# Kernel optimization log

Measured on AMD Instinct MI355X. Metric: run time of the kernel, lower is better.

The kernel has to match this reference:

```python
import jax, jax.numpy as jnp
import numpy as np

D, K, S, H, MID, OUT = 1024, 1024, 1000, 16, 4096, 1000
HD = K // H
EPS = 1e-5


def _posenc(d_model, length):
    pos = jnp.arange(length, dtype=jnp.float32)[:, None]              # [S,1]
    div = jnp.exp(jnp.arange(0, d_model, 2, dtype=jnp.float32) * (-np.log(10000.0) / d_model))
    ang = pos * div                                                   # [S,D/2]
    # interleave sin/cos -> pe[:,0::2]=sin, pe[:,1::2]=cos
    return jnp.stack([jnp.sin(ang), jnp.cos(ang)], axis=-1).reshape(length, d_model)


def _ln2d(x):
    # LayerNorm over last two dims (n_seq, d_dim), no affine
    m = jnp.mean(x, axis=(-2, -1), keepdims=True)
    v = jnp.var(x, axis=(-2, -1), keepdims=True)
    return (x - m) * jax.lax.rsqrt(v + EPS)


def setup_inputs() -> dict:
    key = jax.random.key(0)
    ks = jax.random.split(key, 9)
    sc = lambda fan: 1.0 / np.sqrt(fan)
    return {
        "x":   jax.random.normal(ks[0], (8, S, D), dtype=jnp.float32),
        "Wq":  jax.random.normal(ks[1], (D, K), dtype=jnp.float32) * sc(D),
        "Wk":  jax.random.normal(ks[2], (D, K), dtype=jnp.float32) * sc(D),
        "Wv":  jax.random.normal(ks[3], (D, K), dtype=jnp.float32) * sc(D),
        "Wo":  jax.random.normal(ks[4], (K, D), dtype=jnp.float32) * sc(K),
        "W1":  jax.random.normal(ks[5], (D, MID), dtype=jnp.float32) * sc(D),
        "b1":  jnp.zeros((MID,), dtype=jnp.float32),
        "W2":  jax.random.normal(ks[6], (MID, D), dtype=jnp.float32) * sc(MID),
        "b2":  jnp.zeros((D,), dtype=jnp.float32),
        "Wout": jax.random.normal(ks[7], (D, OUT), dtype=jnp.float32) * sc(D),
    }


def reference(x, Wq, Wk, Wv, Wo, W1, b1, W2, b2, Wout):
    B = x.shape[0]
    x = x + _posenc(D, S)                                   # positional add
    # QKV projections -> [B,H,S,HD]
    def heads(w):
        return jnp.einsum('bsd,dk->bsk', x, w).reshape(B, S, H, HD).transpose(0, 2, 1, 3)
    qs, ksv, vs = heads(Wq), heads(Wk), heads(Wv)
    scaling = HD ** (-0.5)
    scores = jnp.einsum('bhsd,bhtd->bhst', qs, ksv) * scaling
    attn = jax.nn.softmax(scores, axis=-1)
    ctx = jnp.einsum('bhst,bhtd->bhsd', attn, vs)
    ctx = ctx.transpose(0, 2, 1, 3).reshape(B, S, K)
    attn_out = _ln2d(jnp.einsum('bsk,kd->bsd', ctx, Wo))    # per-sample LN over (S,D)
    # FFN with residual + LN over (S,D)
    h = jax.nn.relu(jnp.einsum('bsd,dm->bsm', attn_out, W1) + b1)
    f = jnp.einsum('bsm,md->bsd', h, W2) + b2
    ffn = _ln2d(f + attn_out)
    pooled = jnp.mean(ffn, axis=-2)                         # [B,D]
    return jnp.einsum('bd,do->bo', pooled, Wout)            # [B,OUT]
```

## Files before the change

### kernel.cpp

```cpp
#include <hip/hip_runtime.h>
#include <stdint.h>
#include <math.h>

#define DD 1024
#define SS 1000
#define BB 8
#define HH 16
#define MIDD 4096
#define OUTD 1000

typedef unsigned short u16;
typedef __attribute__((ext_vector_type(4))) float f32x4;
typedef __attribute__((ext_vector_type(4))) unsigned int u32x4;

__device__ __forceinline__ u16 f2b(float f) {
    union { float f; uint32_t u; } v; v.f = f;
    uint32_t r = v.u + 0x7fffu + ((v.u >> 16) & 1u);
    return (u16)(r >> 16);
}
__device__ __forceinline__ float b2f(u16 b) {
    union { uint32_t u; float f; } v; v.u = ((uint32_t)b) << 16; return v.f;
}

__device__ __forceinline__ int sz64(int row, int e) {
    return row * 64 + ((((e >> 3) ^ row) & 7) << 3) + (e & 7);
}

__device__ __forceinline__ void mfma_b16(f32x4& d, u32x4 a, u32x4 b) {
    asm("v_mfma_f32_16x16x32_bf16 %0, %1, %2, %0" : "+v"(d) : "v"(a), "v"(b));
}
#define MFMA_FENCE() do { __builtin_amdgcn_sched_barrier(0); \
    asm volatile("s_nop 7\n\ts_nop 7\n\ts_nop 7" ::); \
    __builtin_amdgcn_sched_barrier(0); } while (0)

#define GLDS16(gp, lp) \
    __builtin_amdgcn_global_load_lds((const __attribute__((address_space(1))) uint32_t*)(gp), \
                                     (__attribute__((address_space(3))) uint32_t*)(lp), 16, 0, 0)

__global__ void k_posenc(const float* __restrict__ x, u16* __restrict__ xpe) {
    long p = (long)blockIdx.x * 256 + threadIdx.x;
    if (p >= (long)BB * SS * DD / 2) return;
    int dp = (int)(p & (DD / 2 - 1));
    int s = (int)((p >> 9) % SS);
    float dv = __expf((float)(2 * dp) * (-9.210340371976184f / (float)DD));
    float sn, cs;
    sincosf((float)s * dv, &sn, &cs);
    float2 xv = *(const float2*)&x[p * 2];
    uint32_t pk = (uint32_t)f2b(xv.x + sn) | ((uint32_t)f2b(xv.y + cs) << 16);
    ((uint32_t*)xpe)[p] = pk;
}

__global__ void k_wt(const float* __restrict__ W, u16* __restrict__ Wt, int R, int C, float scale) {
    __shared__ float tile[32][33];
    int bc = blockIdx.x * 32, br = blockIdx.y * 32;
    int tx = threadIdx.x, ty = threadIdx.y;
#pragma unroll
    for (int i = 0; i < 32; i += 8)
        tile[ty + i][tx] = W[(long)(br + ty + i) * C + bc + tx];
    __syncthreads();
#pragma unroll
    for (int i = 0; i < 32; i += 8)
        Wt[(long)(bc + ty + i) * R + br + tx] = f2b(tile[tx][ty + i] * scale);
}

template<int MODE, int BM, bool NFAST>
__global__ __launch_bounds__(512)
void k_gemm(const u16* __restrict__ A, const u16* __restrict__ Bt, void* __restrict__ Cp,
            const float* __restrict__ bias, const u16* res,
            int M, int N, int K, int lda, int ldb, int ldc, int tiles)
{
    constexpr int MF = BM / 32;
    constexpr int AL = BM / 64;
    constexpr int NBUF = (BM == 128) ? 3 : 2;
    __shared__ u16 SA[NBUF][BM * 64];
    __shared__ u16 SB[NBUF][256 * 64];
    const int t = threadIdx.x, lane = t & 63, w = t >> 6;
    const int lr = lane & 15, g = lane >> 4;
    const int wm = w >> 2, wn = w & 3;

    const int orig = blockIdx.x, nwg = gridDim.x;
    const int q8 = nwg >> 3, r8 = nwg & 7, xc = orig & 7;
    const int wg = (xc < r8 ? xc * (q8 + 1) : r8 * (q8 + 1) + (xc - r8) * q8) + (orig >> 3);
    const int bm = (NFAST ? wg / tiles : wg % tiles) * BM;
    const int bn = (NFAST ? wg % tiles : wg / tiles) * 256;

    const int srow8 = lane >> 3;
    const int csrc = ((lane & 7) ^ srow8) << 3;
    const u16* ga[AL];
    const u16* gb[4];
#pragma unroll
    for (int l = 0; l < AL; ++l) {
        int r = bm + w * (BM / 8) + l * 8 + srow8;
        if (r >= M) r = M - 1;
        ga[l] = A + (long)r * lda + csrc;
    }
#pragma unroll
    for (int l = 0; l < 4; ++l)
        gb[l] = Bt + (long)(bn + w * 32 + l * 8 + srow8) * ldb + csrc;

#define STAGE_A(buf, k0) do { \
        _Pragma("unroll") \
        for (int l = 0; l < AL; ++l) \
            GLDS16(ga[l] + (k0), &SA[buf][(w * (BM / 8) + l * 8) * 64]); \
    } while (0)
#define STAGE_B(buf, k0) do { \
        _Pragma("unroll") \
        for (int l = 0; l < 4; ++l) \
            GLDS16(gb[l] + (k0), &SB[buf][(w * 32 + l * 8) * 64]); \
    } while (0)

    f32x4 acc[MF][4] = {};

#define PH(buf, kk) do { \
        u32x4 av[MF], bv[4]; \
        _Pragma("unroll") \
        for (int m = 0; m < MF; ++m) \
            av[m] = *(const u32x4*)&SA[buf][sz64(wm * (BM / 2) + m * 16 + lr, (kk) * 32 + g * 8)]; \
        _Pragma("unroll") \
        for (int n = 0; n < 4; ++n) \
            bv[n] = *(const u32x4*)&SB[buf][sz64(wn * 64 + n * 16 + lr, (kk) * 32 + g * 8)]; \
        __builtin_amdgcn_s_setprio(1); \
        _Pragma("unroll") \
        for (int m = 0; m < MF; ++m) \
            _Pragma("unroll") \
            for (int n = 0; n < 4; ++n) \
                mfma_b16(acc[m][n], av[m], bv[n]); \
        __builtin_amdgcn_s_setprio(0); \
    } while (0)

    const int nt = K >> 6;

    if constexpr (NBUF == 3) {
        STAGE_A(0, 0); STAGE_B(0, 0);
        STAGE_A(1, 64); STAGE_B(1, 64);
        int cb = 0, sb = 2;
        for (int tt = 0; tt < nt; ++tt) {
            if (tt + 1 < nt) asm volatile("s_waitcnt vmcnt(6)" ::: "memory");
            else             asm volatile("s_waitcnt vmcnt(0)" ::: "memory");
            __builtin_amdgcn_s_barrier();
            if (tt + 2 < nt) { STAGE_A(sb, (tt + 2) << 6); STAGE_B(sb, (tt + 2) << 6); }
            PH(cb, 0);
            PH(cb, 1);
            cb = (cb == 2) ? 0 : cb + 1;
            sb = (sb == 2) ? 0 : sb + 1;
        }
    } else {
        STAGE_A(0, 0); STAGE_B(0, 0);
        for (int tt = 0; tt < nt; ++tt) {
            const int cb2 = tt & 1, nb = cb2 ^ 1, kn = (tt + 1) << 6;
            if (tt + 1 < nt) {
                STAGE_A(nb, kn);
                asm volatile("s_waitcnt vmcnt(4)" ::: "memory");
            } else {
                asm volatile("s_waitcnt vmcnt(0)" ::: "memory");
            }
            __builtin_amdgcn_s_barrier();
            PH(cb2, 0);
            if (tt + 1 < nt) STAGE_B(nb, kn);
            PH(cb2, 1);
            __builtin_amdgcn_s_barrier();
        }
    }
#undef PH
#undef STAGE_A
#undef STAGE_B

    MFMA_FENCE();

#pragma unroll
    for (int m = 0; m < MF; ++m) {
#pragma unroll
        for (int j = 0; j < 4; ++j) {
            const int r = bm + wm * (BM / 2) + m * 16 + g * 4 + j;
            if (r >= M) continue;
            const long ro = (long)r * ldc;
#pragma unroll
            for (int n = 0; n < 4; ++n) {
                const int c = bn + wn * 64 + n * 16 + lr;
                float v = acc[m][n][j];
                if (MODE == 0)      ((float*)Cp)[ro + c] = v;
                else if (MODE == 1) ((u16*)Cp)[ro + c] = f2b(v);
                else if (MODE == 2) { v += bias[c]; ((u16*)Cp)[ro + c] = f2b(v > 0.f ? v : 0.f); }
                else                { v += bias[c] + b2f(res[ro + c]); ((u16*)Cp)[ro + c] = f2b(v); }
            }
        }
    }
}

__global__ void k_vt(const u16* __restrict__ QKV, u16* __restrict__ Vt) {
    __shared__ u16 tile[128][80];
    int b = blockIdx.z, h = blockIdx.y, s0 = blockIdx.x * 128;
    int t = threadIdx.x;
    int rr = t >> 3, cc = (t & 7) * 8;
#pragma unroll
    for (int p = 0; p < 4; ++p) {
        int s = s0 + p * 32 + rr;
        uint4 val = make_uint4(0u, 0u, 0u, 0u);
        if (s < SS) val = *(const uint4*)&QKV[((long)(b * SS + s)) * 3072 + 2048 + h * 64 + cc];
        *(uint4*)&tile[p * 32 + rr][cc] = val;
    }
    __syncthreads();
    int d = t >> 2, sg = (t & 3) * 32;
    long base = ((long)((b * HH + h) * 64 + d)) * 1024 + s0 + sg;
#pragma unroll
    for (int i = 0; i < 4; ++i) {
        u16 tmp[8];
#pragma unroll
        for (int jj = 0; jj < 8; ++jj) tmp[jj] = tile[sg + i * 8 + jj][d];
        *(uint4*)&Vt[base + i * 8] = *(uint4*)tmp;
    }
}

__global__ __launch_bounds__(256)
void k_flash(const u16* __restrict__ QKV, const u16* __restrict__ Vt, u16* __restrict__ ctx)
{
    __shared__ u16 Ps[128 * 64];
    __shared__ u16 Ks[64 * 64];
    __shared__ u16 Vs[64 * 64];
    __shared__ u16 Vones[16 * 64];
    const int t = threadIdx.x, lane = t & 63, wave = t >> 6;
    const int lr = lane & 15, g = lane >> 4;
    const int f = blockIdx.x;
    const int bh = (f & 7) + ((f >> 6) << 3);
    const int q0 = ((f >> 3) & 7) * 128;
    const int h = bh & 15, b = bh >> 4;
    const u16* Qg = QKV + (long)b * SS * 3072 + h * 64;
    const u16* Kg = Qg + 1024;
    const u16* Vg = Vt + (long)bh * 65536;

    const int sr8 = wave * 8 + (lane >> 3);
    const int ssrc = ((lane & 7) ^ (lane >> 3)) * 8;
    const int ldst0 = sr8 * 64 + (lane & 7) * 8;
    const int ldst1 = (32 + sr8) * 64 + (lane & 7) * 8;

#pragma unroll
    for (int r = 0; r < 4; ++r) {
        int qr = q0 + r * 32 + sr8; if (qr >= SS) qr = SS - 1;
        GLDS16(Qg + (long)qr * 3072 + ssrc, &Ps[(r * 32 + wave * 8) * 64]);
    }

    u32x4 kr0, kr1, vr0, vr1;
    {
        kr0 = *(const u32x4*)(Kg + (long)sr8 * 3072 + ssrc);
        kr1 = *(const u32x4*)(Kg + (long)(32 + sr8) * 3072 + ssrc);
        vr0 = *(const u32x4*)(Vg + (long)sr8 * 1024 + ssrc);
        vr1 = *(const u32x4*)(Vg + (long)(32 + sr8) * 1024 + ssrc);
    }

    __syncthreads();
    u32x4 qa[2][2];
#pragma unroll
    for (int m = 0; m < 2; ++m)
#pragma unroll
        for (int ks = 0; ks < 2; ++ks)
            qa[m][ks] = *(const u32x4*)&Ps[sz64(wave * 32 + m * 16 + lr, ks * 32 + g * 8)];

    *(u32x4*)&Ks[ldst0] = kr0;
    *(u32x4*)&Ks[ldst1] = kr1;
    *(u32x4*)&Vs[ldst0] = vr0;
    *(u32x4*)&Vs[ldst1] = vr1;
    for (int i = t; i < 16 * 64; i += 256)
        Vones[sz64(i >> 6, i & 63)] = ((i >> 6) == 0) ? (u16)0x3F80 : (u16)0;
    __syncthreads();

    f32x4 o[2][5] = {};

    for (int tt = 0; tt < 16; ++tt) {
        const int kt = tt * 64;
        if (tt < 15) {
            int a0 = kt + 64 + sr8;      if (a0 >= SS) a0 = SS - 1;
            int a1 = kt + 64 + 32 + sr8; if (a1 >= SS) a1 = SS - 1;
            kr0 = *(const u32x4*)(Kg + (long)a0 * 3072 + ssrc);
            kr1 = *(const u32x4*)(Kg + (long)a1 * 3072 + ssrc);
            vr0 = *(const u32x4*)(Vg + (long)sr8 * 1024 + kt + 64 + ssrc);
            vr1 = *(const u32x4*)(Vg + (long)(32 + sr8) * 1024 + kt + 64 + ssrc);
        }

        f32x4 s[2][4] = {};
#pragma unroll
        for (int ks = 0; ks < 2; ++ks) {
            u32x4 kb[4];
#pragma unroll
            for (int n = 0; n < 4; ++n)
                kb[n] = *(const u32x4*)&Ks[sz64(n * 16 + lr, ks * 32 + g * 8)];
            __builtin_amdgcn_s_setprio(1);
#pragma unroll
            for (int m = 0; m < 2; ++m)
#pragma unroll
                for (int n = 0; n < 4; ++n)
                    mfma_b16(s[m][n], qa[m][ks], kb[n]);
            __builtin_amdgcn_s_setprio(0);
        }
        MFMA_FENCE();

        if (tt == 15) {
#pragma unroll
            for (int n = 0; n < 4; ++n) {
                const bool oob = (kt + n * 16 + lr) >= SS;
                if (oob)
#pragma unroll
                    for (int m = 0; m < 2; ++m)
#pragma unroll
                        for (int j = 0; j < 4; ++j) s[m][n][j] = -1e30f;
            }
        }

#pragma unroll
        for (int m = 0; m < 2; ++m)
#pragma unroll
            for (int j = 0; j < 4; ++j) {
                float p0 = exp2f(s[m][0][j]);
                float p1 = exp2f(s[m][1][j]);
                float p2 = exp2f(s[m][2][j]);
                float p3 = exp2f(s[m][3][j]);
                uint32_t pk01, pk23;
                asm("v_cvt_pk_bf16_f32 %0, %1, %2" : "=v"(pk01) : "v"(p0), "v"(p1));
                asm("v_cvt_pk_bf16_f32 %0, %1, %2" : "=v"(pk23) : "v"(p2), "v"(p3));
                const int prow = wave * 32 + m * 16 + g * 4 + j;
                Ps[sz64(prow, 0 * 16 + lr)] = (u16)(pk01 & 0xffff);
                Ps[sz64(prow, 1 * 16 + lr)] = (u16)(pk01 >> 16);
                Ps[sz64(prow, 2 * 16 + lr)] = (u16)(pk23 & 0xffff);
                Ps[sz64(prow, 3 * 16 + lr)] = (u16)(pk23 >> 16);
            }

        asm volatile("s_waitcnt lgkmcnt(0)" ::: "memory");
        __builtin_amdgcn_sched_barrier(0);

#pragma unroll
        for (int m = 0; m < 2; ++m) {
            u32x4 pa0 = *(const u32x4*)&Ps[sz64(wave * 32 + m * 16 + lr, g * 8)];
            u32x4 pa1 = *(const u32x4*)&Ps[sz64(wave * 32 + m * 16 + lr, 32 + g * 8)];
            __builtin_amdgcn_s_setprio(1);
#pragma unroll
            for (int nd = 0; nd < 4; ++nd) {
                u32x4 vb0 = *(const u32x4*)&Vs[sz64(nd * 16 + lr, g * 8)];
                u32x4 vb1 = *(const u32x4*)&Vs[sz64(nd * 16 + lr, 32 + g * 8)];
                mfma_b16(o[m][nd], pa0, vb0);
                mfma_b16(o[m][nd], pa1, vb1);
            }
            {
                u32x4 vb0 = *(const u32x4*)&Vones[sz64(lr, g * 8)];
                u32x4 vb1 = *(const u32x4*)&Vones[sz64(lr, 32 + g * 8)];
                mfma_b16(o[m][4], pa0, vb0);
                mfma_b16(o[m][4], pa1, vb1);
            }
            __builtin_amdgcn_s_setprio(0);
        }

        if (tt < 15) {
            __syncthreads();
            *(u32x4*)&Ks[ldst0] = kr0;
            *(u32x4*)&Ks[ldst1] = kr1;
            *(u32x4*)&Vs[ldst0] = vr0;
            *(u32x4*)&Vs[ldst1] = vr1;
            __syncthreads();
        }
    }

    MFMA_FENCE();

#pragma unroll
    for (int m = 0; m < 2; ++m)
#pragma unroll
        for (int j = 0; j < 4; ++j) {
            const int r = q0 + wave * 32 + m * 16 + g * 4 + j;
            if (r >= SS) continue;
            const float lval = __shfl(o[m][4][j], lane & 48);
            const float inv = 1.0f / lval;
#pragma unroll
            for (int nd = 0; nd < 4; ++nd)
                ctx[((long)b * SS + r) * 1024 + h * 64 + nd * 16 + lr] = f2b(o[m][nd][j] * inv);
        }
}

__global__ void k_stats1b(const u16* __restrict__ X, float* __restrict__ part) {
    int b = blockIdx.y, blk = blockIdx.x, t = threadIdx.x;
    const uint4* xp = (const uint4*)(X + (long)b * (SS * DD));
    float s = 0.f, q = 0.f;
    for (int i = blk * 256 + t; i < SS * DD / 8; i += 128 * 256) {
        uint4 v = xp[i];
        uint32_t w[4] = { v.x, v.y, v.z, v.w };
#pragma unroll
        for (int jj = 0; jj < 4; ++jj) {
            float a = b2f((u16)(w[jj] & 0xffff)), c = b2f((u16)(w[jj] >> 16));
            s += a + c; q += a * a + c * c;
        }
    }
#pragma unroll
    for (int o = 32; o; o >>= 1) { s += __shfl_xor(s, o, 64); q += __shfl_xor(q, o, 64); }
    __shared__ float rs[4], rq[4];
    if ((t & 63) == 0) { rs[t >> 6] = s; rq[t >> 6] = q; }
    __syncthreads();
    if (t == 0) {
        part[(b * 128 + blk) * 2]     = rs[0] + rs[1] + rs[2] + rs[3];
        part[(b * 128 + blk) * 2 + 1] = rq[0] + rq[1] + rq[2] + rq[3];
    }
}

__global__ void k_stats2(const float* __restrict__ part, float* __restrict__ st) {
    int b = blockIdx.x, t = threadIdx.x;
    float s = part[(b * 128 + t) * 2], q = part[(b * 128 + t) * 2 + 1];
#pragma unroll
    for (int o = 32; o; o >>= 1) { s += __shfl_xor(s, o, 64); q += __shfl_xor(q, o, 64); }
    __shared__ float rs[2], rq[2];
    if ((t & 63) == 0) { rs[t >> 6] = s; rq[t >> 6] = q; }
    __syncthreads();
    if (t == 0) {
        float sm = rs[0] + rs[1], sq = rq[0] + rq[1];
        float mean = sm / (float)(SS * DD);
        float var = sq / (float)(SS * DD) - mean * mean;
        st[b * 2] = mean;
        st[b * 2 + 1] = rsqrtf(var + 1e-5f);
    }
}

__global__ void k_lnapplyb(const u16* __restrict__ X, const float* __restrict__ st,
                           u16* __restrict__ ob) {
    int b = blockIdx.y;
    long i = (long)b * (SS * DD) + ((long)blockIdx.x * 256 + threadIdx.x) * 8;
    const float mean = st[b * 2], rstd = st[b * 2 + 1];
    uint4 v = *(const uint4*)&X[i];
    uint32_t w[4] = { v.x, v.y, v.z, v.w };
    uint32_t r[4];
#pragma unroll
    for (int jj = 0; jj < 4; ++jj) {
        float a = (b2f((u16)(w[jj] & 0xffff)) - mean) * rstd;
        float c = (b2f((u16)(w[jj] >> 16)) - mean) * rstd;
        r[jj] = (uint32_t)f2b(a) | ((uint32_t)f2b(c) << 16);
    }
    *(uint4*)&ob[i] = make_uint4(r[0], r[1], r[2], r[3]);
}

__global__ void k_colpool1(const u16* __restrict__ F, float* __restrict__ partc) {
    int dg = blockIdx.x, sc = blockIdx.y, b = blockIdx.z;
    int d = dg * 256 + threadIdx.x;
    const u16* fp = F + (long)b * (SS * DD) + (long)sc * 125 * DD + d;
    float s = 0.f;
#pragma unroll 5
    for (int i = 0; i < 125; ++i) s += b2f(fp[(long)i * DD]);
    partc[((b * 8 + sc) * DD) + d] = s;
}
__global__ void k_colpool2(const float* __restrict__ partc, const float* __restrict__ st,
                           float* __restrict__ pooled) {
    int b = blockIdx.y, d = blockIdx.x * 256 + threadIdx.x;
    float s = 0.f;
#pragma unroll
    for (int c = 0; c < 8; ++c) s += partc[(b * 8 + c) * DD + d];
    pooled[b * DD + d] = (s * (1.0f / SS) - st[b * 2]) * st[b * 2 + 1];
}

__global__ void k_out1(const float* __restrict__ pooled, const float* __restrict__ Wout,
                       float* __restrict__ po) {
    const int og = blockIdx.x, dc = blockIdx.y, t = threadIdx.x;
    const int o = og * 256 + t;
    __shared__ float pl[8][32];
    pl[t >> 5][t & 31] = pooled[(t >> 5) * DD + dc * 32 + (t & 31)];
    __syncthreads();
    if (o >= OUTD) return;
    float acc[8] = {};
    for (int i = 0; i < 32; ++i) {
        float wv = Wout[(long)(dc * 32 + i) * OUTD + o];
#pragma unroll
        for (int bb = 0; bb < 8; ++bb) acc[bb] = fmaf(pl[bb][i], wv, acc[bb]);
    }
#pragma unroll
    for (int bb = 0; bb < 8; ++bb) po[(dc * 8 + bb) * OUTD + o] = acc[bb];
}
__global__ void k_out2(const float* __restrict__ po, float* __restrict__ out) {
    int b = blockIdx.y, o = blockIdx.x * 256 + threadIdx.x;
    if (o >= OUTD) return;
    float s = 0.f;
    for (int c = 0; c < 32; ++c) s += po[(c * 8 + b) * OUTD + o];
    out[b * OUTD + o] = s;
}

extern "C" void kernel_launch(void* const* d_in, const int* in_sizes, int n_in,
                              void* d_out, int out_size, void* d_ws, size_t ws_size,
                              hipStream_t stream) {
    const float* x    = (const float*)d_in[0];
    const float* Wq   = (const float*)d_in[1];
    const float* Wk   = (const float*)d_in[2];
    const float* Wv   = (const float*)d_in[3];
    const float* Wo   = (const float*)d_in[4];
    const float* W1   = (const float*)d_in[5];
    const float* b1   = (const float*)d_in[6];
    const float* W2   = (const float*)d_in[7];
    const float* b2   = (const float*)d_in[8];
    const float* Wout = (const float*)d_in[9];
    float* out = (float*)d_out;

    char* base = (char*)d_ws;
    u16*   xpe    = (u16*)(base);
    u16*   ctx    = xpe;
    u16*   attnb  = xpe;
    u16*   fout   = xpe;
    u16*   QKVb   = (u16*)(base + 16384000);
    u16*   hb     = QKVb;
    u16*   Vt     = (u16*)(base + 65536000);
    u16*   aob    = Vt;
    float* partc  = (float*)(base + 65536000);
    float* po     = (float*)(base + 65536000 + 262144);
    char*  wbase  = base + 82313216;
    u16*   Wqkvt  = (u16*)(wbase);
    u16*   Wot    = (u16*)(wbase + 6291456);
    u16*   W1t    = (u16*)(wbase + 8388608);
    u16*   W2t    = (u16*)(wbase + 16777216);
    char*  mbase  = base + 107479040;
    float* part   = (float*)(mbase);
    float* st1    = (float*)(mbase + 8192);
    float* st2    = (float*)(mbase + 8448);
    float* pooled = (float*)(mbase + 8704);

    const float CEXP = 0.18033688f;

    dim3 blk(256);
    k_posenc<<<dim3(16000), blk, 0, stream>>>(x, xpe);
    k_wt<<<dim3(32, 32), dim3(32, 8), 0, stream>>>(Wq, Wqkvt, 1024, 1024, CEXP);
    k_wt<<<dim3(32, 32), dim3(32, 8), 0, stream>>>(Wk, Wqkvt + 1048576, 1024, 1024, 1.f);
    k_wt<<<dim3(32, 32), dim3(32, 8), 0, stream>>>(Wv, Wqkvt + 2097152, 1024, 1024, 1.f);
    k_wt<<<dim3(32, 32), dim3(32, 8), 0, stream>>>(Wo, Wot, 1024, 1024, 1.f);
    k_wt<<<dim3(128, 32), dim3(32, 8), 0, stream>>>(W1, W1t, 1024, 4096, 1.f);
    k_wt<<<dim3(32, 128), dim3(32, 8), 0, stream>>>(W2, W2t, 4096, 1024, 1.f);

    k_gemm<1, 128, true><<<dim3(756), dim3(512), 0, stream>>>(xpe, Wqkvt, QKVb, nullptr, nullptr,
                                                              8000, 3072, 1024, 1024, 1024, 3072, 12);
    k_vt<<<dim3(8, 16, 8), blk, 0, stream>>>(QKVb, Vt);

    k_flash<<<dim3(1024), blk, 0, stream>>>(QKVb, Vt, ctx);

    k_gemm<1, 128, true><<<dim3(252), dim3(512), 0, stream>>>(ctx, Wot, aob, nullptr, nullptr,
                                                              8000, 1024, 1024, 1024, 1024, 1024, 4);
    k_stats1b<<<dim3(128, 8), blk, 0, stream>>>(aob, part);
    k_stats2<<<dim3(8), dim3(128), 0, stream>>>(part, st1);
    k_lnapplyb<<<dim3(500, 8), blk, 0, stream>>>(aob, st1, attnb);

    k_gemm<2, 256, false><<<dim3(512), dim3(512), 0, stream>>>(attnb, W1t, hb, b1, nullptr,
                                                               8000, 4096, 1024, 1024, 1024, 4096, 32);
    k_gemm<3, 128, false><<<dim3(252), dim3(512), 0, stream>>>(hb, W2t, fout, b2, attnb,
                                                               8000, 1024, 4096, 4096, 4096, 1024, 63);

    k_stats1b<<<dim3(128, 8), blk, 0, stream>>>(fout, part);
    k_stats2<<<dim3(8), dim3(128), 0, stream>>>(part, st2);
    k_colpool1<<<dim3(4, 8, 8), blk, 0, stream>>>(fout, partc);
    k_colpool2<<<dim3(4, 8), blk, 0, stream>>>(partc, st2, pooled);
    k_out1<<<dim3(4, 32), blk, 0, stream>>>(pooled, Wout, po);
    k_out2<<<dim3(4, 8), blk, 0, stream>>>(po, out);
}
```

Baseline: 435.3 us.

## Add 128x128 four-wave GEMM for N=1024 GEMMs and transpose flash score MFMA

```diff
diff --git a/kernel.cpp b/kernel.cpp
--- a/kernel.cpp
+++ b/kernel.cpp
@@ -36,6 +36,11 @@
 #define GLDS16(gp, lp) \
     __builtin_amdgcn_global_load_lds((const __attribute__((address_space(1))) uint32_t*)(gp), \
                                      (__attribute__((address_space(3))) uint32_t*)(lp), 16, 0, 0)
+
+__device__ __forceinline__ int xcd_swz(int orig, int nwg) {
+    const int q8 = nwg >> 3, r8 = nwg & 7, xc = orig & 7;
+    return (xc < r8 ? xc * (q8 + 1) : r8 * (q8 + 1) + (xc - r8) * q8) + (orig >> 3);
+}
 
 __global__ void k_posenc(const float* __restrict__ x, u16* __restrict__ xpe) {
     long p = (long)blockIdx.x * 256 + threadIdx.x;
@@ -78,9 +83,7 @@
     const int lr = lane & 15, g = lane >> 4;
     const int wm = w >> 2, wn = w & 3;
 
-    const int orig = blockIdx.x, nwg = gridDim.x;
-    const int q8 = nwg >> 3, r8 = nwg & 7, xc = orig & 7;
-    const int wg = (xc < r8 ? xc * (q8 + 1) : r8 * (q8 + 1) + (xc - r8) * q8) + (orig >> 3);
+    const int wg = xcd_swz(blockIdx.x, gridDim.x);
     const int bm = (NFAST ? wg / tiles : wg % tiles) * BM;
     const int bn = (NFAST ? wg % tiles : wg / tiles) * 256;
 
@@ -172,6 +175,107 @@
 #pragma unroll
         for (int j = 0; j < 4; ++j) {
             const int r = bm + wm * (BM / 2) + m * 16 + g * 4 + j;
+            if (r >= M) continue;
+            const long ro = (long)r * ldc;
+#pragma unroll
+            for (int n = 0; n < 4; ++n) {
+                const int c = bn + wn * 64 + n * 16 + lr;
+                float v = acc[m][n][j];
+                if (MODE == 0)      ((float*)Cp)[ro + c] = v;
+                else if (MODE == 1) ((u16*)Cp)[ro + c] = f2b(v);
+                else if (MODE == 2) { v += bias[c]; ((u16*)Cp)[ro + c] = f2b(v > 0.f ? v : 0.f); }
+                else                { v += bias[c] + b2f(res[ro + c]); ((u16*)Cp)[ro + c] = f2b(v); }
+            }
+        }
+    }
+}
+
+template<int MODE, bool NFAST>
+__global__ __launch_bounds__(256)
+void k_gemm4(const u16* __restrict__ A, const u16* __restrict__ Bt, void* __restrict__ Cp,
+             const float* __restrict__ bias, const u16* res,
+             int M, int N, int K, int lda, int ldb, int ldc, int tiles)
+{
+    __shared__ u16 SA[2][128 * 64];
+    __shared__ u16 SB[2][128 * 64];
+    const int t = threadIdx.x, lane = t & 63, w = t >> 6;
+    const int lr = lane & 15, g = lane >> 4;
+    const int wm = w >> 1, wn = w & 1;
+
+    const int wg = xcd_swz(blockIdx.x, gridDim.x);
+    const int bm = (NFAST ? wg / tiles : wg % tiles) * 128;
+    const int bn = (NFAST ? wg % tiles : wg / tiles) * 128;
+
+    const int srow8 = lane >> 3;
+    const int csrc = ((lane & 7) ^ srow8) << 3;
+    const u16* ga[4];
+    const u16* gb[4];
+#pragma unroll
+    for (int l = 0; l < 4; ++l) {
+        int r = bm + w * 32 + l * 8 + srow8;
+        if (r >= M) r = M - 1;
+        ga[l] = A + (long)r * lda + csrc;
+        gb[l] = Bt + (long)(bn + w * 32 + l * 8 + srow8) * ldb + csrc;
+    }
+
+#define STAGE_A(buf, k0) do { \
+        _Pragma("unroll") \
+        for (int l = 0; l < 4; ++l) \
+            GLDS16(ga[l] + (k0), &SA[buf][(w * 32 + l * 8) * 64]); \
+    } while (0)
+#define STAGE_B(buf, k0) do { \
+        _Pragma("unroll") \
+        for (int l = 0; l < 4; ++l) \
+            GLDS16(gb[l] + (k0), &SB[buf][(w * 32 + l * 8) * 64]); \
+    } while (0)
+
+    f32x4 acc[4][4] = {};
+
+#define PH(buf, kk) do { \
+        u32x4 av[4], bv[4]; \
+        _Pragma("unroll") \
+        for (int m = 0; m < 4; ++m) \
+            av[m] = *(const u32x4*)&SA[buf][sz64(wm * 64 + m * 16 + lr, (kk) * 32 + g * 8)]; \
+        _Pragma("unroll") \
+        for (int n = 0; n < 4; ++n) \
+            bv[n] = *(const u32x4*)&SB[buf][sz64(wn * 64 + n * 16 + lr, (kk) * 32 + g * 8)]; \
+        __builtin_amdgcn_s_setprio(1); \
+        _Pragma("unroll") \
+        for (int m = 0; m < 4; ++m) \
+            _Pragma("unroll") \
+            for (int n = 0; n < 4; ++n) \
+                mfma_b16(acc[m][n], av[m], bv[n]); \
+        __builtin_amdgcn_s_setprio(0); \
+    } while (0)
+
+    const int nt = K >> 6;
+
+    STAGE_A(0, 0); STAGE_B(0, 0);
+    for (int tt = 0; tt < nt; ++tt) {
+        const int cb = tt & 1, nb = cb ^ 1, kn = (tt + 1) << 6;
+        if (tt + 1 < nt) {
+            STAGE_A(nb, kn);
+            asm volatile("s_waitcnt vmcnt(4)" ::: "memory");
+        } else {
+            asm volatile("s_waitcnt vmcnt(0)" ::: "memory");
+        }
+        __builtin_amdgcn_s_barrier();
+        PH(cb, 0);
+        if (tt + 1 < nt) STAGE_B(nb, kn);
+        PH(cb, 1);
+        __builtin_amdgcn_s_barrier();
+    }
+#undef PH
+#undef STAGE_A
+#undef STAGE_B
+
+    MFMA_FENCE();
+
+#pragma unroll
+    for (int m = 0; m < 4; ++m) {
+#pragma unroll
+        for (int j = 0; j < 4; ++j) {
+            const int r = bm + wm * 64 + m * 16 + g * 4 + j;
             if (r >= M) continue;
             const long ro = (long)r * ldc;
 #pragma unroll
@@ -276,7 +380,7 @@
             vr1 = *(const u32x4*)(Vg + (long)(32 + sr8) * 1024 + kt + 64 + ssrc);
         }
 
-        f32x4 s[2][4] = {};
+        f32x4 s[4][2] = {};
 #pragma unroll
         for (int ks = 0; ks < 2; ++ks) {
             u32x4 kb[4];
@@ -285,10 +389,10 @@
                 kb[n] = *(const u32x4*)&Ks[sz64(n * 16 + lr, ks * 32 + g * 8)];
             __builtin_amdgcn_s_setprio(1);
 #pragma unroll
-            for (int m = 0; m < 2; ++m)
-#pragma unroll
-                for (int n = 0; n < 4; ++n)
-                    mfma_b16(s[m][n], qa[m][ks], kb[n]);
+            for (int n = 0; n < 4; ++n)
+#pragma unroll
+                for (int m = 0; m < 2; ++m)
+                    mfma_b16(s[n][m], kb[n], qa[m][ks]);
             __builtin_amdgcn_s_setprio(0);
         }
         MFMA_FENCE();
@@ -296,32 +400,28 @@
         if (tt == 15) {
 #pragma unroll
             for (int n = 0; n < 4; ++n) {
-                const bool oob = (kt + n * 16 + lr) >= SS;
-                if (oob)
-#pragma unroll
-                    for (int m = 0; m < 2; ++m)
-#pragma unroll
-                        for (int j = 0; j < 4; ++j) s[m][n][j] = -1e30f;
+                const int kbase = kt + n * 16 + g * 4;
+#pragma unroll
+                for (int j = 0; j < 4; ++j)
+                    if (kbase + j >= SS) { s[n][0][j] = -1e30f; s[n][1][j] = -1e30f; }
             }
         }
 
 #pragma unroll
-        for (int m = 0; m < 2; ++m)
-#pragma unroll
-            for (int j = 0; j < 4; ++j) {
-                float p0 = exp2f(s[m][0][j]);
-                float p1 = exp2f(s[m][1][j]);
-                float p2 = exp2f(s[m][2][j]);
-                float p3 = exp2f(s[m][3][j]);
+        for (int m = 0; m < 2; ++m) {
+            const int prow = wave * 32 + m * 16 + lr;
+#pragma unroll
+            for (int n = 0; n < 4; ++n) {
+                float p0 = exp2f(s[n][m][0]);
+                float p1 = exp2f(s[n][m][1]);
+                float p2 = exp2f(s[n][m][2]);
+                float p3 = exp2f(s[n][m][3]);
                 uint32_t pk01, pk23;
                 asm("v_cvt_pk_bf16_f32 %0, %1, %2" : "=v"(pk01) : "v"(p0), "v"(p1));
                 asm("v_cvt_pk_bf16_f32 %0, %1, %2" : "=v"(pk23) : "v"(p2), "v"(p3));
-                const int prow = wave * 32 + m * 16 + g * 4 + j;
-                Ps[sz64(prow, 0 * 16 + lr)] = (u16)(pk01 & 0xffff);
-                Ps[sz64(prow, 1 * 16 + lr)] = (u16)(pk01 >> 16);
-                Ps[sz64(prow, 2 * 16 + lr)] = (u16)(pk23 & 0xffff);
-                Ps[sz64(prow, 3 * 16 + lr)] = (u16)(pk23 >> 16);
+                *(uint2*)&Ps[sz64(prow, n * 16 + g * 4)] = make_uint2(pk01, pk23);
             }
+        }
 
         asm volatile("s_waitcnt lgkmcnt(0)" ::: "memory");
         __builtin_amdgcn_sched_barrier(0);
@@ -528,16 +628,16 @@
 
     k_flash<<<dim3(1024), blk, 0, stream>>>(QKVb, Vt, ctx);
 
-    k_gemm<1, 128, true><<<dim3(252), dim3(512), 0, stream>>>(ctx, Wot, aob, nullptr, nullptr,
-                                                              8000, 1024, 1024, 1024, 1024, 1024, 4);
+    k_gemm4<1, true><<<dim3(504), blk, 0, stream>>>(ctx, Wot, aob, nullptr, nullptr,
+                                                    8000, 1024, 1024, 1024, 1024, 1024, 8);
     k_stats1b<<<dim3(128, 8), blk, 0, stream>>>(aob, part);
     k_stats2<<<dim3(8), dim3(128), 0, stream>>>(part, st1);
     k_lnapplyb<<<dim3(500, 8), blk, 0, stream>>>(aob, st1, attnb);
 
     k_gemm<2, 256, false><<<dim3(512), dim3(512), 0, stream>>>(attnb, W1t, hb, b1, nullptr,
                                                                8000, 4096, 1024, 1024, 1024, 4096, 32);
-    k_gemm<3, 128, false><<<dim3(252), dim3(512), 0, stream>>>(hb, W2t, fout, b2, attnb,
-                                                               8000, 1024, 4096, 4096, 4096, 1024, 63);
+    k_gemm4<3, false><<<dim3(504), blk, 0, stream>>>(hb, W2t, fout, b2, attnb,
+                                                     8000, 1024, 4096, 4096, 4096, 1024, 63);
 
     k_stats1b<<<dim3(128, 8), blk, 0, stream>>>(fout, part);
     k_stats2<<<dim3(8), dim3(128), 0, stream>>>(part, st2);
```

Result: no change. 430.4 us (-1.1%).
